# Kernel optimization log

Measured on AMD Instinct MI355X. Metric: run time of the kernel, lower is better.

The kernel has to match this reference:

```python
import jax, jax.numpy as jnp
import numpy as np

G_DOWNSAMPLED = 16  # g_downsampled_dimension: tiling factor
XF_DIM = 1024       # xf_dimension
BATCH = 2048


def setup_inputs() -> dict:
    key = jax.random.key(0)
    k1, k2 = jax.random.split(key)
    xf = jax.random.normal(k1, (BATCH, XF_DIM), dtype=jnp.float32)
    wp = jax.random.normal(k2, (1,), dtype=jnp.float32)
    return {"xf": xf, "wp": wp}


def reference(xf, wp):
    # xf_r = relu(xf - mean_batch(xf))
    xf_r = jax.nn.relu(xf - jnp.mean(xf, axis=0))
    # fn_xf = (xf_r - mean(xf_r)) / std(xf_r), std unbiased (torch default ddof=1)
    mu = jnp.mean(xf_r, axis=0)
    sd = jnp.std(xf_r, axis=0, ddof=1)
    fn_xf = (xf_r - mu) / sd
    # matmul with W_tile = kron(ones(1,g), eye(xf_dim)) is an exact tile along features
    x_ = wp * jnp.tile(fn_xf, (1, G_DOWNSAMPLED))  # [batch, g*xf_dim]
    return x_
```

## Files before the change

### kernel.cpp

```cpp
#include <hip/hip_runtime.h>

#define BATCH 2048
#define FDIM  1024
#define GTILE 16
#define F4    (FDIM / 4)
#define CHUNKS 128
#define ROWS_PER_CHUNK (BATCH / CHUNKS)

#define OFF_P1   0
#define OFF_P2S  131072
#define OFF_P2Q  262144
#define OFF_MEAN 393216
#define OFF_SC   394240
#define OFF_CC   395264

__device__ __forceinline__ void v4add(float4& a, const float4& b) {
    a.x += b.x; a.y += b.y; a.z += b.z; a.w += b.w;
}

__global__ void k1_partial_sum(const float4* __restrict__ xf, float4* __restrict__ p1) {
    const int tid = threadIdx.x;
    const int chunk = blockIdx.x;
    const float4* p = xf + (size_t)chunk * ROWS_PER_CHUNK * F4 + tid;
    float4 s = {0.f, 0.f, 0.f, 0.f};
#pragma unroll
    for (int r = 0; r < ROWS_PER_CHUNK; ++r) v4add(s, p[r * F4]);
    p1[chunk * F4 + tid] = s;
}

__global__ void k2_relu_partial(const float4* __restrict__ xf,
                                const float4* __restrict__ p1,
                                float4* __restrict__ p2s,
                                float4* __restrict__ p2q) {
    const int tid = threadIdx.x;
    const int chunk = blockIdx.x;
    float4 m = {0.f, 0.f, 0.f, 0.f};
#pragma unroll 8
    for (int c = 0; c < CHUNKS; ++c) v4add(m, p1[c * F4 + tid]);
    const float inv_n = 1.0f / (float)BATCH;
    m.x *= inv_n; m.y *= inv_n; m.z *= inv_n; m.w *= inv_n;

    const float4* p = xf + (size_t)chunk * ROWS_PER_CHUNK * F4 + tid;
    float4 s = {0.f, 0.f, 0.f, 0.f};
    float4 q = {0.f, 0.f, 0.f, 0.f};
#pragma unroll
    for (int r = 0; r < ROWS_PER_CHUNK; ++r) {
        float4 v = p[r * F4];
        float rx = fmaxf(v.x - m.x, 0.f);
        float ry = fmaxf(v.y - m.y, 0.f);
        float rz = fmaxf(v.z - m.z, 0.f);
        float rw = fmaxf(v.w - m.w, 0.f);
        s.x += rx; s.y += ry; s.z += rz; s.w += rw;
        q.x += rx * rx; q.y += ry * ry; q.z += rz * rz; q.w += rw * rw;
    }
    p2s[chunk * F4 + tid] = s;
    p2q[chunk * F4 + tid] = q;
}

__global__ void k3_finalize(const float* __restrict__ wp,
                            const float4* __restrict__ p1,
                            const float4* __restrict__ p2s,
                            const float4* __restrict__ p2q,
                            float4* __restrict__ mean,
                            float4* __restrict__ sc,
                            float4* __restrict__ cc) {
    __shared__ float4 rm[256], rs[256], rq[256];
    const int t = threadIdx.x;
    const int b = blockIdx.x;
    const int cg = b * 16 + (t & 15);
    const int slice = t >> 4;
    const int c0 = slice * (CHUNKS / 16);
    float4 m = {0.f,0.f,0.f,0.f}, s = {0.f,0.f,0.f,0.f}, q = {0.f,0.f,0.f,0.f};
#pragma unroll
    for (int c = c0; c < c0 + CHUNKS / 16; ++c) {
        v4add(m, p1[c * F4 + cg]);
        v4add(s, p2s[c * F4 + cg]);
        v4add(q, p2q[c * F4 + cg]);
    }
    rm[t] = m; rs[t] = s; rq[t] = q;
    __syncthreads();
    for (int off = 128; off >= 16; off >>= 1) {
        if (t < off) { v4add(rm[t], rm[t + off]); v4add(rs[t], rs[t + off]); v4add(rq[t], rq[t + off]); }
        __syncthreads();
    }
    if (t < 16) {
        const float inv_n = 1.0f / (float)BATCH;
        const float w = wp[0];
        float4 M = rm[t], S = rs[t], Q = rq[t];
        float4 mn, scale, cmb;
        float mu, var;
        mn.x = M.x * inv_n;
        mu = S.x * inv_n; var = (Q.x - S.x * mu) / (float)(BATCH - 1);
        scale.x = w * rsqrtf(var); cmb.x = mu * scale.x;
        mn.y = M.y * inv_n;
        mu = S.y * inv_n; var = (Q.y - S.y * mu) / (float)(BATCH - 1);
        scale.y = w * rsqrtf(var); cmb.y = mu * scale.y;
        mn.z = M.z * inv_n;
        mu = S.z * inv_n; var = (Q.z - S.z * mu) / (float)(BATCH - 1);
        scale.z = w * rsqrtf(var); cmb.z = mu * scale.z;
        mn.w = M.w * inv_n;
        mu = S.w * inv_n; var = (Q.w - S.w * mu) / (float)(BATCH - 1);
        scale.w = w * rsqrtf(var); cmb.w = mu * scale.w;
        mean[b * 16 + t] = mn;
        sc[b * 16 + t]   = scale;
        cc[b * 16 + t]   = cmb;
    }
}

__global__ void k4_write(const float4* __restrict__ xf,
                         const float4* __restrict__ mean,
                         const float4* __restrict__ sc,
                         const float4* __restrict__ cc,
                         float4* __restrict__ out) {
    const int tid = threadIdx.x;
    const int row = blockIdx.x;
    float4 m = mean[tid];
    float4 a = sc[tid];
    float4 c = cc[tid];
    float4 v = xf[(size_t)row * F4 + tid];
    float4 o;
    o.x = fmaxf(v.x - m.x, 0.f) * a.x - c.x;
    o.y = fmaxf(v.y - m.y, 0.f) * a.y - c.y;
    o.z = fmaxf(v.z - m.z, 0.f) * a.z - c.z;
    o.w = fmaxf(v.w - m.w, 0.f) * a.w - c.w;
    float4* dst = out + (size_t)row * (GTILE * F4) + tid;
#pragma unroll
    for (int g = 0; g < GTILE; ++g) {
        dst[g * F4] = o;
    }
}

extern "C" void kernel_launch(void* const* d_in, const int* in_sizes, int n_in,
                              void* d_out, int out_size, void* d_ws, size_t ws_size,
                              hipStream_t stream) {
    const float4* xf4 = (const float4*)d_in[0];
    const float* wp = (const float*)d_in[1];
    float* ws = (float*)d_ws;
    float4* out = (float4*)d_out;

    float4* p1   = (float4*)(ws + OFF_P1);
    float4* p2s  = (float4*)(ws + OFF_P2S);
    float4* p2q  = (float4*)(ws + OFF_P2Q);
    float4* mean = (float4*)(ws + OFF_MEAN);
    float4* sc   = (float4*)(ws + OFF_SC);
    float4* cc   = (float4*)(ws + OFF_CC);

    k1_partial_sum<<<CHUNKS, 256, 0, stream>>>(xf4, p1);
    k2_relu_partial<<<CHUNKS, 256, 0, stream>>>(xf4, p1, p2s, p2q);
    k3_finalize<<<16, 256, 0, stream>>>(wp, p1, p2s, p2q, mean, sc, cc);
    k4_write<<<BATCH, 256, 0, stream>>>(xf4, mean, sc, cc, out);
}
```

Baseline: 155.1 us.

## Fuse relu-stats and finalize kernels into one per-column reduction kernel

Merges the ReLU partial-sum kernel and the finalize kernel into a single kernel with one block per float4 column group. Each block reduces the chunk sums in shared memory to get the mean, then accumulates the ReLU sum and sum of squares and writes scale and offset directly. Chunks are doubled to 256 so each thread covers 8 rows. This drops one launch and the partial-sum round trip through global memory. The cost is that threads in a wave now read different rows of the same column, so the xf loads are strided and poorly coalesced.

```diff
diff --git a/kernel.cpp b/kernel.cpp
--- a/kernel.cpp
+++ b/kernel.cpp
@@ -4,15 +4,13 @@
 #define FDIM  1024
 #define GTILE 16
 #define F4    (FDIM / 4)
-#define CHUNKS 128
+#define CHUNKS 256
 #define ROWS_PER_CHUNK (BATCH / CHUNKS)
 
 #define OFF_P1   0
-#define OFF_P2S  131072
-#define OFF_P2Q  262144
-#define OFF_MEAN 393216
-#define OFF_SC   394240
-#define OFF_CC   395264
+#define OFF_MEAN 262144
+#define OFF_SC   263168
+#define OFF_CC   264192
 
 __device__ __forceinline__ void v4add(float4& a, const float4& b) {
     a.x += b.x; a.y += b.y; a.z += b.z; a.w += b.w;
@@ -28,19 +26,28 @@
     p1[chunk * F4 + tid] = s;
 }
 
-__global__ void k2_relu_partial(const float4* __restrict__ xf,
-                                const float4* __restrict__ p1,
-                                float4* __restrict__ p2s,
-                                float4* __restrict__ p2q) {
-    const int tid = threadIdx.x;
-    const int chunk = blockIdx.x;
-    float4 m = {0.f, 0.f, 0.f, 0.f};
-#pragma unroll 8
-    for (int c = 0; c < CHUNKS; ++c) v4add(m, p1[c * F4 + tid]);
+__global__ void k23_stats(const float4* __restrict__ xf,
+                          const float* __restrict__ wp,
+                          const float4* __restrict__ p1,
+                          float4* __restrict__ mean,
+                          float4* __restrict__ sc,
+                          float4* __restrict__ cc) {
+    __shared__ float4 rA[256], rB[256];
+    const int t = threadIdx.x;
+    const int b = blockIdx.x;
+
+    rA[t] = p1[t * F4 + b];
+    __syncthreads();
+    for (int off = 128; off > 0; off >>= 1) {
+        if (t < off) v4add(rA[t], rA[t + off]);
+        __syncthreads();
+    }
     const float inv_n = 1.0f / (float)BATCH;
+    float4 m = rA[0];
     m.x *= inv_n; m.y *= inv_n; m.z *= inv_n; m.w *= inv_n;
+    if (t == 0) mean[b] = m;
 
-    const float4* p = xf + (size_t)chunk * ROWS_PER_CHUNK * F4 + tid;
+    const float4* p = xf + (size_t)t * ROWS_PER_CHUNK * F4 + b;
     float4 s = {0.f, 0.f, 0.f, 0.f};
     float4 q = {0.f, 0.f, 0.f, 0.f};
 #pragma unroll
@@ -53,57 +60,28 @@
         s.x += rx; s.y += ry; s.z += rz; s.w += rw;
         q.x += rx * rx; q.y += ry * ry; q.z += rz * rz; q.w += rw * rw;
     }
-    p2s[chunk * F4 + tid] = s;
-    p2q[chunk * F4 + tid] = q;
-}
-
-__global__ void k3_finalize(const float* __restrict__ wp,
-                            const float4* __restrict__ p1,
-                            const float4* __restrict__ p2s,
-                            const float4* __restrict__ p2q,
-                            float4* __restrict__ mean,
-                            float4* __restrict__ sc,
-                            float4* __restrict__ cc) {
-    __shared__ float4 rm[256], rs[256], rq[256];
-    const int t = threadIdx.x;
-    const int b = blockIdx.x;
-    const int cg = b * 16 + (t & 15);
-    const int slice = t >> 4;
-    const int c0 = slice * (CHUNKS / 16);
-    float4 m = {0.f,0.f,0.f,0.f}, s = {0.f,0.f,0.f,0.f}, q = {0.f,0.f,0.f,0.f};
-#pragma unroll
-    for (int c = c0; c < c0 + CHUNKS / 16; ++c) {
-        v4add(m, p1[c * F4 + cg]);
-        v4add(s, p2s[c * F4 + cg]);
-        v4add(q, p2q[c * F4 + cg]);
-    }
-    rm[t] = m; rs[t] = s; rq[t] = q;
     __syncthreads();
-    for (int off = 128; off >= 16; off >>= 1) {
-        if (t < off) { v4add(rm[t], rm[t + off]); v4add(rs[t], rs[t + off]); v4add(rq[t], rq[t + off]); }
+    rA[t] = s; rB[t] = q;
+    __syncthreads();
+    for (int off = 128; off > 0; off >>= 1) {
+        if (t < off) { v4add(rA[t], rA[t + off]); v4add(rB[t], rB[t + off]); }
         __syncthreads();
     }
-    if (t < 16) {
-        const float inv_n = 1.0f / (float)BATCH;
+    if (t == 0) {
         const float w = wp[0];
-        float4 M = rm[t], S = rs[t], Q = rq[t];
-        float4 mn, scale, cmb;
+        float4 S = rA[0], Q = rB[0];
+        float4 scale, cmb;
         float mu, var;
-        mn.x = M.x * inv_n;
         mu = S.x * inv_n; var = (Q.x - S.x * mu) / (float)(BATCH - 1);
         scale.x = w * rsqrtf(var); cmb.x = mu * scale.x;
-        mn.y = M.y * inv_n;
         mu = S.y * inv_n; var = (Q.y - S.y * mu) / (float)(BATCH - 1);
         scale.y = w * rsqrtf(var); cmb.y = mu * scale.y;
-        mn.z = M.z * inv_n;
         mu = S.z * inv_n; var = (Q.z - S.z * mu) / (float)(BATCH - 1);
         scale.z = w * rsqrtf(var); cmb.z = mu * scale.z;
-        mn.w = M.w * inv_n;
         mu = S.w * inv_n; var = (Q.w - S.w * mu) / (float)(BATCH - 1);
         scale.w = w * rsqrtf(var); cmb.w = mu * scale.w;
-        mean[b * 16 + t] = mn;
-        sc[b * 16 + t]   = scale;
-        cc[b * 16 + t]   = cmb;
+        sc[b] = scale;
+        cc[b] = cmb;
     }
 }
 
@@ -139,14 +117,11 @@
     float4* out = (float4*)d_out;
 
     float4* p1   = (float4*)(ws + OFF_P1);
-    float4* p2s  = (float4*)(ws + OFF_P2S);
-    float4* p2q  = (float4*)(ws + OFF_P2Q);
     float4* mean = (float4*)(ws + OFF_MEAN);
     float4* sc   = (float4*)(ws + OFF_SC);
     float4* cc   = (float4*)(ws + OFF_CC);
 
     k1_partial_sum<<<CHUNKS, 256, 0, stream>>>(xf4, p1);
-    k2_relu_partial<<<CHUNKS, 256, 0, stream>>>(xf4, p1, p2s, p2q);
-    k3_finalize<<<16, 256, 0, stream>>>(wp, p1, p2s, p2q, mean, sc, cc);
+    k23_stats<<<F4, 256, 0, stream>>>(xf4, wp, p1, mean, sc, cc);
     k4_write<<<BATCH, 256, 0, stream>>>(xf4, mean, sc, cc, out);
 }
```

New measurement: 157.8 us. No clear change (+1.7%).
